# Performance work log

Hardware: AMD Instinct MI355X
Metric: run time of the kernel (lower is better)

The kernel has to match this reference:

```python
import jax, jax.numpy as jnp
import numpy as np

B, L, H, NH = 4, 512, 512, 8
DK = H // NH
REPR_IN, REPR_HID = 53, 32
EPS = 1e-5


def setup_inputs() -> dict:
    key = jax.random.key(0)
    ks = jax.random.split(key, 12)
    x = jax.random.normal(ks[0], (B, L, H), dtype=jnp.float32)
    mask = jax.random.randint(ks[1], (B, L), 0, 2, dtype=jnp.int32)
    refCov = jax.random.normal(ks[2], (B, L, L, REPR_IN), dtype=jnp.float32)
    def lin(k, fan_in, fan_out):
        return jax.random.normal(k, (fan_in, fan_out), dtype=jnp.float32) / np.sqrt(fan_in)
    Wv = lin(ks[3], H, H); bv = jnp.zeros((H,), jnp.float32)
    W1 = lin(ks[4], REPR_IN, REPR_HID); b1 = jnp.zeros((REPR_HID,), jnp.float32)
    W2 = lin(ks[5], REPR_HID, NH); b2 = jnp.zeros((NH,), jnp.float32)
    Wo = lin(ks[6], H, H); bo = jnp.zeros((H,), jnp.float32)
    gamma = jnp.ones((H,), jnp.float32); beta = jnp.zeros((H,), jnp.float32)
    return {"x": x, "mask": mask, "refCov": refCov, "Wv": Wv, "bv": bv,
            "W1": W1, "b1": b1, "W2": W2, "b2": b2, "Wo": Wo, "bo": bo,
            "gamma": gamma, "beta": beta}


def reference(x, mask, refCov, Wv, bv, W1, b1, W2, b2, Wo, bo, gamma, beta):
    Bx, Lx, Hx = x.shape
    residual = x
    # value projection -> (B, NH, L, DK)
    value = (x @ Wv + bv).reshape(Bx, Lx, NH, DK).transpose(0, 2, 1, 3)
    # per-pair MLP on refCov: (B, L, L, 53) -> (B, L, L, NH)
    h1 = jax.nn.relu(refCov @ W1 + b1)
    scores = jnp.transpose(h1 @ W2 + b2, (0, 3, 1, 2))  # (B, NH, L, L)
    # pairwise mask and softmax
    m = mask.astype(bool)
    mask2d = m[:, :, None] & m[:, None, :]              # (B, L, L)
    masked = jnp.where(mask2d[:, None, :, :], scores, -jnp.inf)
    all_inf_rows = ~jnp.any(mask2d, axis=-1)            # (B, L) rows fully masked
    masked = jnp.where(all_inf_rows[:, None, :, None], 0.0, masked)
    attn = jax.nn.softmax(masked, axis=-1)
    # weighted sum and output projection
    out = jnp.einsum('bhij,bhjd->bhid', attn, value)
    out = out.transpose(0, 2, 1, 3).reshape(Bx, Lx, Hx)
    out = out @ Wo + bo
    # residual + LayerNorm
    y = residual + out
    mu = jnp.mean(y, axis=-1, keepdims=True)
    var = jnp.var(y, axis=-1, keepdims=True)
    return (y - mu) / jnp.sqrt(var + EPS) * gamma + beta
```

## Files before the change

### kernel.cpp

```cpp
#include <hip/hip_runtime.h>
#include <hip/hip_bf16.h>
#include <math.h>

#define B 4
#define L 512
#define H 512
#define NH 8
#define DK 64
#define RIN 53
#define RHID 32

using short8 = __attribute__((ext_vector_type(8))) short;
using ushort8v = __attribute__((ext_vector_type(8))) unsigned short;
using f32x4 = __attribute__((ext_vector_type(4))) float;

__device__ __forceinline__ unsigned short cvt_bf16(float f) {
  __hip_bfloat16 h = __float2bfloat16(f);
  return __builtin_bit_cast(unsigned short, h);
}
__device__ __forceinline__ float bf2f(unsigned short u) {
  return __uint_as_float((unsigned)u << 16);
}

__global__ __launch_bounds__(512) void prep_kernel(
    const int* __restrict__ mask, int* __restrict__ jidx, int* __restrict__ nv,
    const float* __restrict__ Wv, const float* __restrict__ Wo,
    unsigned short* __restrict__ WvT, unsigned short* __restrict__ WoT) {
  const int bid = blockIdx.x;
  const int tid = threadIdx.x;
  if (bid < 4) {
    const int b = bid;
    const int lane = tid & 63, wv = tid >> 6;
    __shared__ int wtot[8], woff[8];
    const int m = (mask[b * 512 + tid] != 0);
    const unsigned long long bal = __ballot(m);
    const int lpre = __popcll(bal & ((1ull << lane) - 1ull));
    if (lane == 0) wtot[wv] = __popcll(bal);
    __syncthreads();
    if (tid == 0) {
      int acc = 0;
#pragma unroll
      for (int q = 0; q < 8; ++q) {
        woff[q] = acc;
        acc += wtot[q];
      }
      nv[b] = acc;
    }
    __syncthreads();
    if (m) jidx[b * 512 + woff[wv] + lpre] = tid;
    return;
  }
  const int t = bid - 4;
  const int matsel = t >> 6;
  const int tile = t & 63;
  const float* W = matsel ? Wo : Wv;
  unsigned short* WT = matsel ? WoT : WvT;
  const int k0 = (tile & 7) * 64, n0 = (tile >> 3) * 64;
  __shared__ float sT[64][65];
  {
    const int r = tid >> 3, c0 = (tid & 7) * 8;
    const float4 v0 = *(const float4*)(W + (size_t)(k0 + r) * 512 + n0 + c0);
    const float4 v1 = *(const float4*)(W + (size_t)(k0 + r) * 512 + n0 + c0 + 4);
    sT[r][c0] = v0.x; sT[r][c0 + 1] = v0.y; sT[r][c0 + 2] = v0.z; sT[r][c0 + 3] = v0.w;
    sT[r][c0 + 4] = v1.x; sT[r][c0 + 5] = v1.y; sT[r][c0 + 6] = v1.z; sT[r][c0 + 7] = v1.w;
  }
  __syncthreads();
  {
    const int n = tid >> 3, c0 = (tid & 7) * 8;
    ushort8v o;
#pragma unroll
    for (int cc = 0; cc < 8; ++cc) o[cc] = cvt_bf16(sT[c0 + cc][n]);
    *(ushort8v*)(WT + (size_t)(n0 + n) * 512 + k0 + c0) = o;
  }
}

template <int AMODE, int OMODE, int BK>
__device__ __forceinline__ void gemm32x64(
    char* __restrict__ smem, const void* __restrict__ Aq, int lda,
    const unsigned short* __restrict__ Bs, int ldb,
    const float* __restrict__ bias, void* __restrict__ Cp, int ldc) {
  constexpr int KS = BK / 8;
  constexpr int STR = BK + 8;
  constexpr int NA = 32 * KS / 256;
  constexpr int NB = 64 * KS / 256;
  unsigned short* sA = (unsigned short*)smem;
  unsigned short* sB = (unsigned short*)(smem + 32 * STR * 2);
  float(*sC)[68] = (float(*)[68])smem;
  const int tid = threadIdx.x;
  const int w = tid >> 6, l = tid & 63, g = l >> 4, a = l & 15;
  const int wm = (w >> 1) * 16, wn = (w & 1) * 32;
  f32x4 acc0 = {}, acc1 = {};

  ushort8v aR[NA], bR[NB];
  auto loadA = [&](int k0) {
#pragma unroll
    for (int q = 0; q < NA; ++q) {
      const int s = tid + q * 256;
      const int row = s / KS, kk = s % KS;
      if constexpr (AMODE == 1) {
        const float* Af = (const float*)Aq;
        const float* p = Af + (size_t)row * lda + k0 + kk * 8;
        const float4 v0 = *(const float4*)p;
        const float4 v1 = *(const float4*)(p + 4);
        ushort8v r;
        r[0] = cvt_bf16(v0.x); r[1] = cvt_bf16(v0.y);
        r[2] = cvt_bf16(v0.z); r[3] = cvt_bf16(v0.w);
        r[4] = cvt_bf16(v1.x); r[5] = cvt_bf16(v1.y);
        r[6] = cvt_bf16(v1.z); r[7] = cvt_bf16(v1.w);
        aR[q] = r;
      } else {
        const unsigned short* Ab = (const unsigned short*)Aq;
        aR[q] = *(const ushort8v*)(Ab + (size_t)row * lda + k0 + kk * 8);
      }
    }
  };
  auto loadB = [&](int k0) {
#pragma unroll
    for (int q = 0; q < NB; ++q) {
      const int s = tid + q * 256;
      const int row = s / KS, kk = s % KS;
      bR[q] = *(const ushort8v*)(Bs + (size_t)row * ldb + k0 + kk * 8);
    }
  };
  auto stage = [&]() {
#pragma unroll
    for (int q = 0; q < NA; ++q) {
      const int s = tid + q * 256;
      *(ushort8v*)(&sA[(s / KS) * STR + (s % KS) * 8]) = aR[q];
    }
#pragma unroll
    for (int q = 0; q < NB; ++q) {
      const int s = tid + q * 256;
      *(ushort8v*)(&sB[(s / KS) * STR + (s % KS) * 8]) = bR[q];
    }
  };

  loadA(0);
  loadB(0);
  for (int k0 = 0; k0 < 512; k0 += BK) {
    stage();
    __syncthreads();
    if (k0 + BK < 512) {
      loadA(k0 + BK);
      loadB(k0 + BK);
    }
#pragma unroll
    for (int ks = 0; ks < BK / 32; ++ks) {
      const short8 af = *(const short8*)(&sA[(wm + a) * STR + ks * 32 + g * 8]);
      const short8 bf0 = *(const short8*)(&sB[(wn + a) * STR + ks * 32 + g * 8]);
      const short8 bf1 =
          *(const short8*)(&sB[(wn + 16 + a) * STR + ks * 32 + g * 8]);
      acc0 = __builtin_amdgcn_mfma_f32_16x16x32_bf16(af, bf0, acc0, 0, 0, 0);
      acc1 = __builtin_amdgcn_mfma_f32_16x16x32_bf16(af, bf1, acc1, 0, 0, 0);
    }
    __syncthreads();
  }

#pragma unroll
  for (int r = 0; r < 4; ++r) {
    sC[wm + g * 4 + r][wn + a] = acc0[r];
    sC[wm + g * 4 + r][wn + 16 + a] = acc1[r];
  }
  __syncthreads();

  if constexpr (OMODE == 2) {
    const int n = tid >> 2, iq = (tid & 3) * 8;
    const float bv = bias ? bias[n] : 0.f;
    ushort8v o;
#pragma unroll
    for (int cc = 0; cc < 8; ++cc) o[cc] = cvt_bf16(sC[iq + cc][n] + bv);
    *(ushort8v*)((unsigned short*)Cp + (size_t)n * ldc + iq) = o;
  } else {
    const int m = tid >> 3, c8 = (tid & 7) * 8;
    float v[8];
#pragma unroll
    for (int cc = 0; cc < 8; ++cc) {
      v[cc] = sC[m][c8 + cc];
      if (bias) v[cc] += bias[c8 + cc];
    }
    if constexpr (OMODE == 1) {
      ushort8v o;
#pragma unroll
      for (int cc = 0; cc < 8; ++cc) o[cc] = cvt_bf16(v[cc]);
      *(ushort8v*)((unsigned short*)Cp + (size_t)m * ldc + c8) = o;
    } else {
      *(float4*)((float*)Cp + (size_t)m * ldc + c8) =
          make_float4(v[0], v[1], v[2], v[3]);
      *(float4*)((float*)Cp + (size_t)m * ldc + c8 + 4) =
          make_float4(v[4], v[5], v[6], v[7]);
    }
  }
}

#define GEMM64_SMEM 13824
#define GEMM128_SMEM 26112

#define FUSED_SMEM 15616
__global__ __launch_bounds__(256) void fused_scores_value_kernel(
    const float* __restrict__ refCov, const int* __restrict__ mask,
    const int* __restrict__ jidx, const int* __restrict__ nvArr,
    const float* __restrict__ W1, const float* __restrict__ b1,
    const float* __restrict__ W2, const float* __restrict__ b2,
    unsigned short* __restrict__ attnb, const float* __restrict__ x,
    const unsigned short* __restrict__ WvT, const float* __restrict__ bv,
    unsigned short* __restrict__ valT) {
  __shared__ __align__(16) char smem[FUSED_SMEM];
  const int tid = threadIdx.x;

  if (blockIdx.x >= 2048) {
    const int gb = blockIdx.x - 2048;
    const int n0 = (gb & 7) * 64;
    const int m0 = (gb >> 3) * 32;
    const int b = m0 >> 9, i0 = m0 & 511;
    gemm32x64<1, 2, 64>(smem, x + (size_t)m0 * 512, 512,
                        WvT + (size_t)n0 * 512, 512, bv + n0,
                        valT + (size_t)b * 262144 + (size_t)n0 * 512 + i0, 512);
    return;
  }

  unsigned short* sH1 = (unsigned short*)smem;
  int* sJ = (int*)(smem + 5120);
  unsigned short* sOut = (unsigned short*)(smem + 7168);
  float(*redbuf)[16] = (float(*)[16])(smem + 15360);

  const int b = blockIdx.x >> 9;
  const int i = blockIdx.x & (L - 1);
  const int w = tid >> 6;
  const int l = tid & 63;
  const int g = l >> 4;
  const int a = l & 15;

  const int mi = mask[b * L + i];
  const int nv = nvArr[b];

  if (mi == 0 || nv == 0) {
    const ushort4 u4 = {0x3B00u, 0x3B00u, 0x3B00u, 0x3B00u};
#pragma unroll
    for (int q = 0; q < 4; ++q) {
      const int f4 = q * 256 + tid;
      const int h = f4 >> 7;
      const int c4 = f4 & 127;
      *(ushort4*)(attnb + ((size_t)(b * NH + h) * L + i) * L + c4 * 4) = u4;
    }
    return;
  }

  sJ[tid] = jidx[b * 512 + tid];
  sJ[tid + 256] = jidx[b * 512 + 256 + tid];

  short8 w1f[2][2];
#pragma unroll
  for (int ks = 0; ks < 2; ++ks)
#pragma unroll
    for (int nt = 0; nt < 2; ++nt)
#pragma unroll
      for (int e = 0; e < 8; ++e) {
        const int k = ks * 32 + g * 8 + e;
        w1f[ks][nt][e] =
            (k < RIN) ? (short)cvt_bf16(W1[k * RHID + nt * 16 + a]) : (short)0;
      }
  short8 w2f;
#pragma unroll
  for (int e = 0; e < 8; ++e) {
    const int k = g * 8 + e;
    w2f[e] = (a < NH) ? (short)cvt_bf16(W2[k * NH + a]) : (short)0;
  }
  const float b1v0 = b1[a];
  const float b1v1 = b1[16 + a];
  const float b2v = (a < NH) ? b2[a] : 0.f;

  __syncthreads();

  const int NT = (nv + 15) >> 4;
  f32x4 sc[8];

#pragma unroll
  for (int mt = 0; mt < 8; ++mt) {
    const int t = mt * 4 + w;
    if (t >= NT) continue;
    const int s = t * 16 + a;
    const int j = sJ[(s < nv) ? s : (nv - 1)];
    const float* rp = refCov + ((size_t)((b << 9) + i) * 512 + j) * RIN;

    const float4 u0 = *(const float4*)(rp + g * 8);
    const float4 u1 = *(const float4*)(rp + g * 8 + 4);
    const int base0 = (g < 3) ? (32 + g * 8) : 32;
    const int base1 = (g == 0) ? 36 : (g == 1) ? 44 : 49;
    const float4 v0 = *(const float4*)(rp + base0);
    const float4 v1 = *(const float4*)(rp + base1);
    float t1[8];
    if (g < 3) {
      t1[0] = v0.x; t1[1] = v0.y; t1[2] = v0.z; t1[3] = v0.w;
    } else {
      t1[0] = 0.f; t1[1] = 0.f; t1[2] = 0.f; t1[3] = 0.f;
    }
    if (g < 2) {
      t1[4] = v1.x; t1[5] = v1.y; t1[6] = v1.z; t1[7] = v1.w;
    } else if (g == 2) {
      t1[4] = v1.w;
      t1[5] = 0.f; t1[6] = 0.f; t1[7] = 0.f;
    } else {
      t1[4] = 0.f; t1[5] = 0.f; t1[6] = 0.f; t1[7] = 0.f;
    }
    short8 af0, af1;
    af0[0] = (short)cvt_bf16(u0.x); af0[1] = (short)cvt_bf16(u0.y);
    af0[2] = (short)cvt_bf16(u0.z); af0[3] = (short)cvt_bf16(u0.w);
    af0[4] = (short)cvt_bf16(u1.x); af0[5] = (short)cvt_bf16(u1.y);
    af0[6] = (short)cvt_bf16(u1.z); af0[7] = (short)cvt_bf16(u1.w);
#pragma unroll
    for (int e = 0; e < 8; ++e) af1[e] = (short)cvt_bf16(t1[e]);

    f32x4 h0 = f32x4{b1v0, b1v0, b1v0, b1v0};
    f32x4 h1v = f32x4{b1v1, b1v1, b1v1, b1v1};
    h0 = __builtin_amdgcn_mfma_f32_16x16x32_bf16(af0, w1f[0][0], h0, 0, 0, 0);
    h1v = __builtin_amdgcn_mfma_f32_16x16x32_bf16(af0, w1f[0][1], h1v, 0, 0, 0);
    h0 = __builtin_amdgcn_mfma_f32_16x16x32_bf16(af1, w1f[1][0], h0, 0, 0, 0);
    h1v = __builtin_amdgcn_mfma_f32_16x16x32_bf16(af1, w1f[1][1], h1v, 0, 0, 0);

#pragma unroll
    for (int r = 0; r < 4; ++r) {
      sH1[(w * 16 + g * 4 + r) * 40 + a] = cvt_bf16(fmaxf(h0[r], 0.f));
      sH1[(w * 16 + g * 4 + r) * 40 + 16 + a] = cvt_bf16(fmaxf(h1v[r], 0.f));
    }

    const short8 af2 = *(const short8*)(&sH1[(w * 16 + a) * 40 + g * 8]);
    f32x4 acc = f32x4{b2v, b2v, b2v, b2v};
    sc[mt] = __builtin_amdgcn_mfma_f32_16x16x32_bf16(af2, w2f, acc, 0, 0, 0);
  }

  float mx = -INFINITY;
#pragma unroll
  for (int mt = 0; mt < 8; ++mt) {
    const int t = mt * 4 + w;
    if (t >= NT) continue;
#pragma unroll
    for (int r = 0; r < 4; ++r) {
      const int s = t * 16 + g * 4 + r;
      if (s < nv) mx = fmaxf(mx, sc[mt][r]);
    }
  }
  mx = fmaxf(mx, __shfl_xor(mx, 16, 64));
  mx = fmaxf(mx, __shfl_xor(mx, 32, 64));
  if (g == 0) redbuf[w][a] = mx;
  __syncthreads();
  const float rmax = fmaxf(fmaxf(redbuf[0][a], redbuf[1][a]),
                           fmaxf(redbuf[2][a], redbuf[3][a]));
  __syncthreads();

  float lsum = 0.f;
#pragma unroll
  for (int mt = 0; mt < 8; ++mt) {
    const int t = mt * 4 + w;
    if (t >= NT) continue;
#pragma unroll
    for (int r = 0; r < 4; ++r) {
      const int s = t * 16 + g * 4 + r;
      const float e = (s < nv) ? __expf(sc[mt][r] - rmax) : 0.f;
      sc[mt][r] = e;
      lsum += e;
    }
  }
  lsum += __shfl_xor(lsum, 16, 64);
  lsum += __shfl_xor(lsum, 32, 64);
  if (g == 0) redbuf[w][a] = lsum;
  __syncthreads();
  const float rsum = redbuf[0][a] + redbuf[1][a] + redbuf[2][a] + redbuf[3][a];
  const float inv = 1.f / rsum;

  {
    const ushort8v z{};
    *(ushort8v*)(&sOut[tid * 16]) = z;
    *(ushort8v*)(&sOut[tid * 16 + 8]) = z;
  }
  __syncthreads();
  if (a < NH) {
#pragma unroll
    for (int mt = 0; mt < 8; ++mt) {
      const int t = mt * 4 + w;
      if (t >= NT) continue;
#pragma unroll
      for (int r = 0; r < 4; ++r) {
        const int s = t * 16 + g * 4 + r;
        if (s < nv) sOut[a * 512 + sJ[s]] = cvt_bf16(sc[mt][r] * inv);
      }
    }
  }
  __syncthreads();
  {
    const int h = tid >> 5, off = (tid & 31) * 16;
    unsigned short* dst = attnb + ((size_t)(b * NH + h) * L + i) * L + off;
    *(ushort8v*)dst = *(const ushort8v*)(&sOut[h * 512 + off]);
    *(ushort8v*)(dst + 8) = *(const ushort8v*)(&sOut[h * 512 + off + 8]);
  }
}

__global__ __launch_bounds__(256) void attn_value_kernel(
    const unsigned short* __restrict__ attnb,
    const unsigned short* __restrict__ valT, unsigned short* __restrict__ ctx) {
  __shared__ __align__(16) char smem[GEMM128_SMEM];
  const int bid = blockIdx.x;
  const int it = bid & 15, h = (bid >> 4) & 7, b = bid >> 7;
  const int i0 = it * 32;
  gemm32x64<0, 1, 128>(smem, attnb + ((size_t)((b * 8 + h) * 512 + i0)) * 512,
                       512, valT + (size_t)b * 262144 + (size_t)(h * 64) * 512,
                       512, nullptr,
                       ctx + ((size_t)(b * 512 + i0)) * 512 + h * 64, 512);
}

__global__ __launch_bounds__(256) void gemm_proj_kernel(
    const unsigned short* __restrict__ ctx,
    const unsigned short* __restrict__ WoT, const float* __restrict__ bo,
    unsigned short* __restrict__ proj) {
  __shared__ __align__(16) char smem[GEMM128_SMEM];
  const int n0 = blockIdx.x * 64;
  const int m0 = blockIdx.y * 32;
  gemm32x64<0, 1, 128>(smem, ctx + (size_t)m0 * 512, 512,
                       WoT + (size_t)n0 * 512, 512, bo + n0,
                       proj + (size_t)m0 * 512 + n0, 512);
}

__global__ __launch_bounds__(256) void residual_ln_kernel(
    const float* __restrict__ x, const unsigned short* __restrict__ proj,
    const float* __restrict__ gamma, const float* __restrict__ beta,
    float* __restrict__ out) {
  const int tid = threadIdx.x;
  const int rh = tid >> 7;
  const int q = tid & 127;
  const int row = blockIdx.x * 2 + rh;
  __shared__ float redS[4], redQ[4];

  const float4 xv = *(const float4*)(x + (size_t)row * H + q * 4);
  const ushort4 pv = *(const ushort4*)(proj + (size_t)row * H + q * 4);
  float y[4] = {xv.x + bf2f(pv.x), xv.y + bf2f(pv.y), xv.z + bf2f(pv.z),
                xv.w + bf2f(pv.w)};
  float ls = y[0] + y[1] + y[2] + y[3];
  float lq = y[0] * y[0] + y[1] * y[1] + y[2] * y[2] + y[3] * y[3];
#pragma unroll
  for (int off = 32; off > 0; off >>= 1) {
    ls += __shfl_xor(ls, off, 64);
    lq += __shfl_xor(lq, off, 64);
  }
  const int wave = tid >> 6, lane = tid & 63;
  if (lane == 0) {
    redS[wave] = ls;
    redQ[wave] = lq;
  }
  __syncthreads();
  const float sum = redS[rh * 2] + redS[rh * 2 + 1];
  const float sq = redQ[rh * 2] + redQ[rh * 2 + 1];
  const float mu = sum * (1.f / H);
  const float var = sq * (1.f / H) - mu * mu;
  const float inv = rsqrtf(var + 1e-5f);
  const float4 gm = *(const float4*)(gamma + q * 4);
  const float4 bt = *(const float4*)(beta + q * 4);
  float4 o;
  o.x = (y[0] - mu) * inv * gm.x + bt.x;
  o.y = (y[1] - mu) * inv * gm.y + bt.y;
  o.z = (y[2] - mu) * inv * gm.z + bt.z;
  o.w = (y[3] - mu) * inv * gm.w + bt.w;
  *(float4*)(out + (size_t)row * H + q * 4) = o;
}

extern "C" void kernel_launch(void* const* d_in, const int* in_sizes, int n_in,
                              void* d_out, int out_size, void* d_ws,
                              size_t ws_size, hipStream_t stream) {
  const float* x = (const float*)d_in[0];
  const int* mask = (const int*)d_in[1];
  const float* refCov = (const float*)d_in[2];
  const float* Wv = (const float*)d_in[3];
  const float* bv = (const float*)d_in[4];
  const float* W1 = (const float*)d_in[5];
  const float* b1 = (const float*)d_in[6];
  const float* W2 = (const float*)d_in[7];
  const float* b2 = (const float*)d_in[8];
  const float* Wo = (const float*)d_in[9];
  const float* bo = (const float*)d_in[10];
  const float* gamma = (const float*)d_in[11];
  const float* beta = (const float*)d_in[12];
  float* out = (float*)d_out;

  const size_t n_attn = (size_t)B * NH * L * L;
  const size_t n_blh = (size_t)B * L * H;
  const size_t n_w = (size_t)H * H;
  unsigned short* attnb = (unsigned short*)d_ws;
  unsigned short* valT = attnb + n_attn;
  unsigned short* ctx = valT + n_blh;
  unsigned short* WvT = ctx + n_blh;
  unsigned short* WoT = WvT + n_w;
  unsigned short* proj = WoT + n_w;
  int* jidx = (int*)(proj + n_blh);
  int* nv = jidx + B * L;
  const size_t needed =
      (n_attn + 3 * n_blh + 2 * n_w) * 2 + (B * L + B) * 4;
  if (ws_size < needed) return;

  const int M = B * L;

  prep_kernel<<<132, 512, 0, stream>>>(mask, jidx, nv, Wv, Wo, WvT, WoT);
  fused_scores_value_kernel<<<2048 + 512, 256, 0, stream>>>(
      refCov, mask, jidx, nv, W1, b1, W2, b2, attnb, x, WvT, bv, valT);
  attn_value_kernel<<<512, 256, 0, stream>>>(attnb, valT, ctx);
  gemm_proj_kernel<<<dim3(8, M / 32), 256, 0, stream>>>(ctx, WoT, bo, proj);
  residual_ln_kernel<<<M / 2, 256, 0, stream>>>(x, proj, gamma, beta, out);
}
```

Measured before the change: 59.27 us.

## Compact attention to valid keys and bound PV GEMM K-loop by valid count

Value rows are now gathered by the compacted valid-key index, and attention probabilities are stored in compacted order, so the attention-times-value GEMM only loops over K up to the valid count rounded to 128. Fully masked query rows (whose softmax is uniform over all keys) are replaced by a precomputed mean of V, built from a column sum of x in the prep kernel and a matvec in extra blocks. This removes work on masked keys but adds two serial reduction phases: a 512-step column loop per thread and a slow per-thread matvec over WvT.

```diff
diff --git a/kernel.cpp b/kernel.cpp
--- a/kernel.cpp
+++ b/kernel.cpp
@@ -25,7 +25,8 @@
 __global__ __launch_bounds__(512) void prep_kernel(
     const int* __restrict__ mask, int* __restrict__ jidx, int* __restrict__ nv,
     const float* __restrict__ Wv, const float* __restrict__ Wo,
-    unsigned short* __restrict__ WvT, unsigned short* __restrict__ WoT) {
+    unsigned short* __restrict__ WvT, unsigned short* __restrict__ WoT,
+    const float* __restrict__ x, float* __restrict__ xsum) {
   const int bid = blockIdx.x;
   const int tid = threadIdx.x;
   if (bid < 4) {
@@ -50,6 +51,13 @@
     if (m) jidx[b * 512 + woff[wv] + lpre] = tid;
     return;
   }
+  if (bid >= 132) {
+    const int b = bid - 132;
+    float acc = 0.f;
+    for (int j = 0; j < 512; ++j) acc += x[((size_t)(b * 512) + j) * 512 + tid];
+    xsum[b * 512 + tid] = acc;
+    return;
+  }
   const int t = bid - 4;
   const int matsel = t >> 6;
   const int tile = t & 63;
@@ -78,7 +86,9 @@
 __device__ __forceinline__ void gemm32x64(
     char* __restrict__ smem, const void* __restrict__ Aq, int lda,
     const unsigned short* __restrict__ Bs, int ldb,
-    const float* __restrict__ bias, void* __restrict__ Cp, int ldc) {
+    const float* __restrict__ bias, void* __restrict__ Cp, int ldc,
+    int kend = 512, const int* __restrict__ maskRow = nullptr,
+    const float* __restrict__ meanVslice = nullptr, bool alldead = false) {
   constexpr int KS = BK / 8;
   constexpr int STR = BK + 8;
   constexpr int NA = 32 * KS / 256;
@@ -98,8 +108,7 @@
       const int s = tid + q * 256;
       const int row = s / KS, kk = s % KS;
       if constexpr (AMODE == 1) {
-        const float* Af = (const float*)Aq;
-        const float* p = Af + (size_t)row * lda + k0 + kk * 8;
+        const float* p = (const float*)Aq + k0 + kk * 8;
         const float4 v0 = *(const float4*)p;
         const float4 v1 = *(const float4*)(p + 4);
         ushort8v r;
@@ -135,12 +144,14 @@
     }
   };
 
-  loadA(0);
-  loadB(0);
-  for (int k0 = 0; k0 < 512; k0 += BK) {
+  if (kend > 0) {
+    loadA(0);
+    loadB(0);
+  }
+  for (int k0 = 0; k0 < kend; k0 += BK) {
     stage();
     __syncthreads();
-    if (k0 + BK < 512) {
+    if (k0 + BK < kend) {
       loadA(k0 + BK);
       loadB(k0 + BK);
     }
@@ -172,23 +183,16 @@
     *(ushort8v*)((unsigned short*)Cp + (size_t)n * ldc + iq) = o;
   } else {
     const int m = tid >> 3, c8 = (tid & 7) * 8;
-    float v[8];
+    const bool dead = alldead || (maskRow && maskRow[m] == 0);
+    ushort8v o;
 #pragma unroll
     for (int cc = 0; cc < 8; ++cc) {
-      v[cc] = sC[m][c8 + cc];
-      if (bias) v[cc] += bias[c8 + cc];
-    }
-    if constexpr (OMODE == 1) {
-      ushort8v o;
-#pragma unroll
-      for (int cc = 0; cc < 8; ++cc) o[cc] = cvt_bf16(v[cc]);
-      *(ushort8v*)((unsigned short*)Cp + (size_t)m * ldc + c8) = o;
-    } else {
-      *(float4*)((float*)Cp + (size_t)m * ldc + c8) =
-          make_float4(v[0], v[1], v[2], v[3]);
-      *(float4*)((float*)Cp + (size_t)m * ldc + c8 + 4) =
-          make_float4(v[4], v[5], v[6], v[7]);
-    }
+      float v = sC[m][c8 + cc];
+      if (bias) v += bias[c8 + cc];
+      if (maskRow && dead) v = meanVslice[c8 + cc];
+      o[cc] = cvt_bf16(v);
+    }
+    *(ushort8v*)((unsigned short*)Cp + (size_t)m * ldc + c8) = o;
   }
 }
 
@@ -203,18 +207,43 @@
     const float* __restrict__ W2, const float* __restrict__ b2,
     unsigned short* __restrict__ attnb, const float* __restrict__ x,
     const unsigned short* __restrict__ WvT, const float* __restrict__ bv,
-    unsigned short* __restrict__ valT) {
+    unsigned short* __restrict__ valT, const float* __restrict__ xsum,
+    float* __restrict__ meanV) {
   __shared__ __align__(16) char smem[FUSED_SMEM];
   const int tid = threadIdx.x;
+
+  if (blockIdx.x >= 2560) {
+    const int b = blockIdx.x - 2560;
+    float* sX = (float*)smem;
+    sX[tid] = xsum[b * 512 + tid];
+    sX[tid + 256] = xsum[b * 512 + 256 + tid];
+    __syncthreads();
+#pragma unroll
+    for (int p = 0; p < 2; ++p) {
+      const int n = tid * 2 + p;
+      float acc = 0.f;
+      for (int kc = 0; kc < 64; ++kc) {
+        const ushort8v wv = *(const ushort8v*)(WvT + (size_t)n * 512 + kc * 8);
+#pragma unroll
+        for (int e = 0; e < 8; ++e) acc += sX[kc * 8 + e] * bf2f(wv[e]);
+      }
+      meanV[b * 512 + n] = acc * (1.f / 512.f) + bv[n];
+    }
+    return;
+  }
 
   if (blockIdx.x >= 2048) {
     const int gb = blockIdx.x - 2048;
     const int n0 = (gb & 7) * 64;
     const int m0 = (gb >> 3) * 32;
-    const int b = m0 >> 9, i0 = m0 & 511;
-    gemm32x64<1, 2, 64>(smem, x + (size_t)m0 * 512, 512,
-                        WvT + (size_t)n0 * 512, 512, bv + n0,
-                        valT + (size_t)b * 262144 + (size_t)n0 * 512 + i0, 512);
+    const int b = m0 >> 9, s0 = m0 & 511;
+    const int nvb = nvArr[b];
+    const int row = tid >> 3;
+    const int s = s0 + row;
+    const int srcj = (s < nvb) ? jidx[b * 512 + s] : 0;
+    const float* arow = x + ((size_t)(b * 512) + srcj) * 512;
+    gemm32x64<1, 2, 64>(smem, arow, 512, WvT + (size_t)n0 * 512, 512, bv + n0,
+                        valT + (size_t)b * 262144 + (size_t)n0 * 512 + s0, 512);
     return;
   }
 
@@ -232,15 +261,17 @@
 
   const int mi = mask[b * L + i];
   const int nv = nvArr[b];
+  const int kend = (nv + 127) & ~127;
 
   if (mi == 0 || nv == 0) {
-    const ushort4 u4 = {0x3B00u, 0x3B00u, 0x3B00u, 0x3B00u};
-#pragma unroll
-    for (int q = 0; q < 4; ++q) {
-      const int f4 = q * 256 + tid;
-      const int h = f4 >> 7;
-      const int c4 = f4 & 127;
-      *(ushort4*)(attnb + ((size_t)(b * NH + h) * L + i) * L + c4 * 4) = u4;
+    if (kend > 0) {
+      const ushort8v z{};
+      const int h = tid >> 5, off = (tid & 31) * 16;
+      if (off < kend) {
+        unsigned short* dst = attnb + ((size_t)(b * NH + h) * L + i) * L + off;
+        *(ushort8v*)dst = z;
+        *(ushort8v*)(dst + 8) = z;
+      }
     }
     return;
   }
@@ -381,30 +412,38 @@
 #pragma unroll
       for (int r = 0; r < 4; ++r) {
         const int s = t * 16 + g * 4 + r;
-        if (s < nv) sOut[a * 512 + sJ[s]] = cvt_bf16(sc[mt][r] * inv);
+        if (s < nv) sOut[a * 512 + s] = cvt_bf16(sc[mt][r] * inv);
       }
     }
   }
   __syncthreads();
   {
     const int h = tid >> 5, off = (tid & 31) * 16;
-    unsigned short* dst = attnb + ((size_t)(b * NH + h) * L + i) * L + off;
-    *(ushort8v*)dst = *(const ushort8v*)(&sOut[h * 512 + off]);
-    *(ushort8v*)(dst + 8) = *(const ushort8v*)(&sOut[h * 512 + off + 8]);
+    if (off < kend) {
+      unsigned short* dst = attnb + ((size_t)(b * NH + h) * L + i) * L + off;
+      *(ushort8v*)dst = *(const ushort8v*)(&sOut[h * 512 + off]);
+      *(ushort8v*)(dst + 8) = *(const ushort8v*)(&sOut[h * 512 + off + 8]);
+    }
   }
 }
 
 __global__ __launch_bounds__(256) void attn_value_kernel(
     const unsigned short* __restrict__ attnb,
-    const unsigned short* __restrict__ valT, unsigned short* __restrict__ ctx) {
+    const unsigned short* __restrict__ valT, const int* __restrict__ mask,
+    const int* __restrict__ nvArr, const float* __restrict__ meanV,
+    unsigned short* __restrict__ ctx) {
   __shared__ __align__(16) char smem[GEMM128_SMEM];
   const int bid = blockIdx.x;
   const int it = bid & 15, h = (bid >> 4) & 7, b = bid >> 7;
   const int i0 = it * 32;
+  const int nvb = nvArr[b];
+  const int kend = (nvb + 127) & ~127;
   gemm32x64<0, 1, 128>(smem, attnb + ((size_t)((b * 8 + h) * 512 + i0)) * 512,
                        512, valT + (size_t)b * 262144 + (size_t)(h * 64) * 512,
                        512, nullptr,
-                       ctx + ((size_t)(b * 512 + i0)) * 512 + h * 64, 512);
+                       ctx + ((size_t)(b * 512 + i0)) * 512 + h * 64, 512, kend,
+                       mask + b * 512 + i0, meanV + b * 512 + h * 64,
+                       nvb == 0);
 }
 
 __global__ __launch_bounds__(256) void gemm_proj_kernel(
@@ -490,16 +529,20 @@
   unsigned short* proj = WoT + n_w;
   int* jidx = (int*)(proj + n_blh);
   int* nv = jidx + B * L;
-  const size_t needed =
-      (n_attn + 3 * n_blh + 2 * n_w) * 2 + (B * L + B) * 4;
+  float* xsum = (float*)(nv + B);
+  float* meanV = xsum + B * H;
+  const size_t needed = (n_attn + 3 * n_blh + 2 * n_w) * 2 +
+                        (B * L + B) * 4 + 2 * B * H * 4;
   if (ws_size < needed) return;
 
   const int M = B * L;
 
-  prep_kernel<<<132, 512, 0, stream>>>(mask, jidx, nv, Wv, Wo, WvT, WoT);
-  fused_scores_value_kernel<<<2048 + 512, 256, 0, stream>>>(
-      refCov, mask, jidx, nv, W1, b1, W2, b2, attnb, x, WvT, bv, valT);
-  attn_value_kernel<<<512, 256, 0, stream>>>(attnb, valT, ctx);
+  prep_kernel<<<136, 512, 0, stream>>>(mask, jidx, nv, Wv, Wo, WvT, WoT, x,
+                                       xsum);
+  fused_scores_value_kernel<<<2564, 256, 0, stream>>>(
+      refCov, mask, jidx, nv, W1, b1, W2, b2, attnb, x, WvT, bv, valT, xsum,
+      meanV);
+  attn_value_kernel<<<512, 256, 0, stream>>>(attnb, valT, mask, nv, meanV, ctx);
   gemm_proj_kernel<<<dim3(8, M / 32), 256, 0, stream>>>(ctx, WoT, bo, proj);
   residual_ln_kernel<<<M / 2, 256, 0, stream>>>(x, proj, gamma, beta, out);
 }
```

Result: slower. 81.10 us (+36.8%).
